# Kernel tuning notes

Measured on AMD Instinct MI355X. Metric: run time of the kernel, lower is better.

Reference implementation:

```python
import jax, jax.numpy as jnp
import numpy as np

B, S, E, H = 64, 512, 1024, 1024

def setup_inputs() -> dict:
    key = jax.random.key(0)
    k1, k2, k3, k4, k5 = jax.random.split(key, 5)
    emben_x = jax.random.normal(k1, (B, S, E), dtype=jnp.float32)
    sW = 1.0 / np.sqrt(E)
    sU = 1.0 / np.sqrt(H)
    W_w = jax.random.uniform(k2, (H, E), jnp.float32, -sW, sW)
    W_b = jax.random.uniform(k3, (H,), jnp.float32, -sW, sW)
    U_w = jax.random.uniform(k4, (H, H), jnp.float32, -sU, sU)
    U_b = jax.random.uniform(k5, (H,), jnp.float32, -sU, sU)
    return {"emben_x": emben_x, "W_w": W_w, "W_b": W_b, "U_w": U_w, "U_b": U_b}

def reference(emben_x, W_w, W_b, U_w, U_b):
    # Precompute input projection for all timesteps in one big GEMM: [B,S,H]
    wx = jnp.einsum('bse,he->bsh', emben_x, W_w) + W_b

    def step(t, wx_t):
        # h3 = tanh(W x_t + b_W + t); t_new = U h3 + b_U
        h3 = jnp.tanh(wx_t + t)
        t_new = h3 @ U_w.T + U_b
        return t_new, t_new

    t0 = jnp.zeros((emben_x.shape[0], U_w.shape[0]), dtype=emben_x.dtype)
    t_final, outs = jax.lax.scan(step, t0, jnp.swapaxes(wx, 0, 1))  # outs: [S,B,H]
    result1 = jnp.swapaxes(outs, 0, 1)  # [B,S,H]
    return result1, t_final
```

## Files before the change

kernel.cpp:

```cpp
#include <hip/hip_runtime.h>
#include <hip/hip_bf16.h>
#include <math.h>

#define RB 64
#define RS 512
#define RE 1024
#define RH 1024
#define BSH ((size_t)RB * RS * RH)

#define NBLK 256

typedef __attribute__((ext_vector_type(8))) __bf16 bf16x8;
typedef __attribute__((ext_vector_type(4))) float  f32x4;

__device__ __forceinline__ bf16x8 cvt8(f32x4 a, f32x4 b) {
    bf16x8 r;
    r[0] = (__bf16)a[0]; r[1] = (__bf16)a[1];
    r[2] = (__bf16)a[2]; r[3] = (__bf16)a[3];
    r[4] = (__bf16)b[0]; r[5] = (__bf16)b[1];
    r[6] = (__bf16)b[2]; r[7] = (__bf16)b[3];
    return r;
}

__device__ __forceinline__ bf16x8 ld_frag_agent(const unsigned long long* p) {
    union { unsigned long long u[2]; bf16x8 v; } r;
    r.u[0] = __hip_atomic_load(p,     __ATOMIC_RELAXED, __HIP_MEMORY_SCOPE_AGENT);
    r.u[1] = __hip_atomic_load(p + 1, __ATOMIC_RELAXED, __HIP_MEMORY_SCOPE_AGENT);
    return r.v;
}
__device__ __forceinline__ void st_bf16_agent(__bf16* p, float v) {
    union { __bf16 b; unsigned short s; } u;
    u.b = (__bf16)v;
    __hip_atomic_store(reinterpret_cast<unsigned short*>(p), u.s,
                       __ATOMIC_RELAXED, __HIP_MEMORY_SCOPE_AGENT);
}

__global__ void init_flags_k(unsigned* flags) {
    if (threadIdx.x < NBLK) flags[threadIdx.x] = 0u;
}

#define WBK  64
#define LDST 72

__global__ __launch_bounds__(256) void wx_gemm(
    const float* __restrict__ X,
    const float* __restrict__ Ww,
    const float* __restrict__ Wb,
    float* __restrict__ Out)
{
    __shared__ __align__(16) __bf16 As[128 * LDST];
    __shared__ __align__(16) __bf16 Bs[128 * LDST];

    const int tid  = threadIdx.x;
    const int lane = tid & 63;
    const int wave = tid >> 6;
    const int m0   = blockIdx.y * 128;
    const int n0   = blockIdx.x * 128;
    const int wm   = (wave >> 1) * 64;
    const int wn   = (wave & 1) * 64;

    const int sk   = (tid & 7) * 8;
    const int srow = tid >> 3;

    f32x4 acc[4][4];
#pragma unroll
    for (int i = 0; i < 4; ++i)
#pragma unroll
        for (int j = 0; j < 4; ++j) acc[i][j] = (f32x4){0.f, 0.f, 0.f, 0.f};

    for (int kc = 0; kc < RE; kc += WBK) {
#pragma unroll
        for (int rr = 0; rr < 128; rr += 32) {
            const float* xp = X + (size_t)(m0 + srow + rr) * RE + kc + sk;
            *reinterpret_cast<bf16x8*>(&As[(srow + rr) * LDST + sk]) =
                cvt8(*reinterpret_cast<const f32x4*>(xp),
                     *reinterpret_cast<const f32x4*>(xp + 4));
            const float* wp = Ww + (size_t)(n0 + srow + rr) * RE + kc + sk;
            *reinterpret_cast<bf16x8*>(&Bs[(srow + rr) * LDST + sk]) =
                cvt8(*reinterpret_cast<const f32x4*>(wp),
                     *reinterpret_cast<const f32x4*>(wp + 4));
        }
        __syncthreads();

#pragma unroll
        for (int ks = 0; ks < 2; ++ks) {
            bf16x8 af[4], bfr[4];
#pragma unroll
            for (int i = 0; i < 4; ++i) {
                af[i]  = *reinterpret_cast<const bf16x8*>(
                    &As[(wm + i * 16 + (lane & 15)) * LDST + ks * 32 + (lane >> 4) * 8]);
                bfr[i] = *reinterpret_cast<const bf16x8*>(
                    &Bs[(wn + i * 16 + (lane & 15)) * LDST + ks * 32 + (lane >> 4) * 8]);
            }
#pragma unroll
            for (int i = 0; i < 4; ++i)
#pragma unroll
                for (int j = 0; j < 4; ++j)
                    acc[i][j] = __builtin_amdgcn_mfma_f32_16x16x32_bf16(
                        af[i], bfr[j], acc[i][j], 0, 0, 0);
        }
        __syncthreads();
    }

    const int col = lane & 15, rbase = (lane >> 4) * 4;
#pragma unroll
    for (int j = 0; j < 4; ++j) {
        const int n = n0 + wn + j * 16 + col;
        const float bias = Wb[n];
#pragma unroll
        for (int i = 0; i < 4; ++i) {
#pragma unroll
            for (int r = 0; r < 4; ++r) {
                const int m = m0 + wm + i * 16 + rbase + r;
                Out[(size_t)m * RH + n] = acc[i][j][r] + bias;
            }
        }
    }
}

__global__ __launch_bounds__(128) void rnn_scan(
    const float* __restrict__ Uw,
    const float* __restrict__ Ub,
    float* Out,
    __bf16* hbuf,
    unsigned* flags)
{
    __shared__ float red[2][2][256];

    const int tid  = threadIdx.x;
    const int lane = tid & 63;
    const int wave = tid >> 6;
    const int bid  = blockIdx.x;
    const int cg   = bid >> 2;
    const int rg   = bid & 3;
    const int col0 = cg * 16;
    const int row0 = rg * 16;
    const int slot = rg * 64 + cg;

    bf16x8 ufr[16];
    {
        const float* up = Uw + (size_t)(col0 + (lane & 15)) * RH
                        + 512 * wave + ((lane >> 4) * 8);
#pragma unroll
        for (int j = 0; j < 16; ++j)
            ufr[j] = cvt8(*reinterpret_cast<const f32x4*>(up + j * 32),
                          *reinterpret_cast<const f32x4*>(up + j * 32 + 4));
    }

    const int e0row = row0 + (tid >> 4);
    const int e1row = e0row + 8;
    const int ecol  = col0 + (tid & 15);
    const float ub  = Ub[ecol];

    {
        const float w0 = Out[(size_t)e0row * RS * RH + ecol];
        const float w1 = Out[(size_t)e1row * RS * RH + ecol];
        st_bf16_agent(hbuf + e0row * RH + ecol, tanhf(w0));
        st_bf16_agent(hbuf + e1row * RH + ecol, tanhf(w1));
    }
    __syncthreads();
    if (tid == 0)
        __hip_atomic_store(&flags[slot], 1u,
                           __ATOMIC_RELAXED, __HIP_MEMORY_SCOPE_AGENT);

    const int arow  = row0 + (lane & 15);
    const int kbase = 512 * wave + (lane >> 4) * 8;
    const unsigned* myflags = flags + rg * 64;

    for (int t = 0; t < RS; ++t) {
        const __bf16* cur = hbuf + (size_t)(t & 1) * (RB * RH);
        __bf16*       nxt = hbuf + (size_t)((t + 1) & 1) * (RB * RH);
        const unsigned long long* cp =
            reinterpret_cast<const unsigned long long*>(cur)
            + ((size_t)arow * RH + kbase) / 4;

        float wn0 = 0.f, wn1 = 0.f;
        if (t < RS - 1) {
            wn0 = Out[(size_t)e0row * RS * RH + (size_t)(t + 1) * RH + ecol];
            wn1 = Out[(size_t)e1row * RS * RH + (size_t)(t + 1) * RH + ecol];
        }

        const unsigned tgt = (unsigned)(t + 1);
        while (true) {
            const unsigned f = __hip_atomic_load(&myflags[lane],
                                                 __ATOMIC_RELAXED,
                                                 __HIP_MEMORY_SCOPE_AGENT);
            if (__all(f >= tgt)) break;
            __builtin_amdgcn_s_sleep(1);
        }
        __builtin_amdgcn_sched_barrier(0);
        asm volatile("" ::: "memory");

        bf16x8 x[16];
#pragma unroll
        for (int f = 0; f < 16; ++f)
            x[f] = ld_frag_agent(cp + f * 8);

        f32x4 ac0 = (f32x4){0.f, 0.f, 0.f, 0.f};
        f32x4 ac1 = ac0, ac2 = ac0, ac3 = ac0;
#pragma unroll
        for (int f = 0; f < 16; f += 4) {
            ac0 = __builtin_amdgcn_mfma_f32_16x16x32_bf16(x[f + 0], ufr[f + 0], ac0, 0, 0, 0);
            ac1 = __builtin_amdgcn_mfma_f32_16x16x32_bf16(x[f + 1], ufr[f + 1], ac1, 0, 0, 0);
            ac2 = __builtin_amdgcn_mfma_f32_16x16x32_bf16(x[f + 2], ufr[f + 2], ac2, 0, 0, 0);
            ac3 = __builtin_amdgcn_mfma_f32_16x16x32_bf16(x[f + 3], ufr[f + 3], ac3, 0, 0, 0);
        }
        const f32x4 acc = (ac0 + ac1) + (ac2 + ac3);

        {
            float* rb = red[t & 1][wave];
#pragma unroll
            for (int r = 0; r < 4; ++r)
                rb[((lane >> 4) * 4 + r) * 16 + (lane & 15)] = acc[r];
        }
        __syncthreads();
        const float* r0 = red[t & 1][0];
        const float* r1 = red[t & 1][1];
        const float v0 = r0[tid]       + r1[tid]       + ub;
        const float v1 = r0[tid + 128] + r1[tid + 128] + ub;

        const size_t o0 = (size_t)e0row * RS * RH + (size_t)t * RH + ecol;
        const size_t o1 = (size_t)e1row * RS * RH + (size_t)t * RH + ecol;
        if (t == RS - 1) {
            Out[o0] = v0;
            Out[o1] = v1;
            Out[BSH + (size_t)e0row * RH + ecol] = v0;
            Out[BSH + (size_t)e1row * RH + ecol] = v1;
        } else {
            st_bf16_agent(nxt + e0row * RH + ecol, tanhf(wn0 + v0));
            st_bf16_agent(nxt + e1row * RH + ecol, tanhf(wn1 + v1));
            __syncthreads();
            if (tid == 0)
                __hip_atomic_store(&flags[slot], (unsigned)(t + 2),
                                   __ATOMIC_RELAXED, __HIP_MEMORY_SCOPE_AGENT);
            Out[o0] = v0;
            Out[o1] = v1;
        }
    }
}

extern "C" void kernel_launch(void* const* d_in, const int* in_sizes, int n_in,
                              void* d_out, int out_size, void* d_ws, size_t ws_size,
                              hipStream_t stream)
{
    const float* X  = (const float*)d_in[0];
    const float* Ww = (const float*)d_in[1];
    const float* Wb = (const float*)d_in[2];
    const float* Uw = (const float*)d_in[3];
    const float* Ub = (const float*)d_in[4];
    float* Out = (float*)d_out;

    __bf16* hbuf = (__bf16*)d_ws;
    unsigned* flags = (unsigned*)((char*)d_ws + (size_t)2 * RB * RH * sizeof(__bf16));

    hipLaunchKernelGGL(init_flags_k, dim3(1), dim3(256), 0, stream, flags);
    hipLaunchKernelGGL(wx_gemm, dim3(RH / 128, (RB * RS) / 128), dim3(256), 0, stream,
                       X, Ww, Wb, Out);
    hipLaunchKernelGGL(rnn_scan, dim3(NBLK), dim3(128), 0, stream,
                       Uw, Ub, Out, hbuf, flags);
}
```

Baseline: 2.245 ms.

## Replace per-step flag barrier with timestep-tagged hidden-state words in RNN scan

Adds a new scan kernel in which each hidden value is stored as a 32-bit word that packs the bf16 value with the timestep in the upper half. Consumers spin until every word they need carries the expected tag, so the separate flag handshake between producer and consumer blocks goes away. The block also grows to 4 waves splitting K four ways, with a shared-memory reduction. The cost is twice the bytes of hidden-state traffic and a full re-read whenever a tag check fails. The old flag-based path is kept as a fallback for when the workspace is too small.

```diff
diff --git a/kernel.cpp b/kernel.cpp
--- a/kernel.cpp
+++ b/kernel.cpp
@@ -33,6 +33,12 @@
     u.b = (__bf16)v;
     __hip_atomic_store(reinterpret_cast<unsigned short*>(p), u.s,
                        __ATOMIC_RELAXED, __HIP_MEMORY_SCOPE_AGENT);
+}
+
+__global__ __launch_bounds__(256) void init_tags_k(unsigned* tbuf) {
+    const int i = blockIdx.x * 256 + threadIdx.x;
+    tbuf[i]         = 0xFFFF0000u;
+    tbuf[i + 65536] = 0xFFFF0000u;
 }
 
 __global__ void init_flags_k(unsigned* flags) {
@@ -118,7 +124,135 @@
     }
 }
 
-__global__ __launch_bounds__(128) void rnn_scan(
+__global__ __launch_bounds__(256) void rnn_scan_tag(
+    const float* __restrict__ Uw,
+    const float* __restrict__ Ub,
+    float* Out,
+    unsigned* tbuf)
+{
+    __shared__ float red[2][4 * 256];
+    __shared__ float ubs[16];
+
+    const int tid  = threadIdx.x;
+    const int lane = tid & 63;
+    const int wave = tid >> 6;
+    const int bid  = blockIdx.x;
+    const int cg   = bid >> 2;
+    const int rg   = bid & 3;
+    const int col0 = cg * 16;
+    const int row0 = rg * 16;
+
+    bf16x8 ufr[8];
+    {
+        const float* up = Uw + (size_t)(col0 + (lane & 15)) * RH
+                        + 256 * wave + ((lane >> 4) * 8);
+#pragma unroll
+        for (int j = 0; j < 8; ++j)
+            ufr[j] = cvt8(*reinterpret_cast<const f32x4*>(up + j * 32),
+                          *reinterpret_cast<const f32x4*>(up + j * 32 + 4));
+    }
+    if (tid < 16) ubs[tid] = Ub[col0 + tid];
+
+    const int erow = row0 + (tid >> 4);
+    const int ecol = col0 + (tid & 15);
+
+    {
+        const float w = Out[(size_t)erow * RS * RH + ecol];
+        union { __bf16 b; unsigned short s; } u; u.b = (__bf16)tanhf(w);
+        __hip_atomic_store(&tbuf[(size_t)erow * RH + ecol], (unsigned)u.s,
+                           __ATOMIC_RELAXED, __HIP_MEMORY_SCOPE_AGENT);
+    }
+    float wn_cur = Out[(size_t)erow * RS * RH + (size_t)1 * RH + ecol];
+
+    const int arow  = row0 + (lane & 15);
+    const int kbase = 256 * wave + (lane >> 4) * 8;
+
+    for (int t = 0; t < RS; ++t) {
+        const unsigned* cur = tbuf + (size_t)(t & 1) * (RB * RH);
+        unsigned*       nxt = tbuf + (size_t)((t + 1) & 1) * (RB * RH);
+        const unsigned long long* cp =
+            reinterpret_cast<const unsigned long long*>(cur)
+            + ((size_t)arow * RH + kbase) / 2;
+
+        const unsigned long long half = ((unsigned long long)(unsigned)t) << 16;
+        const unsigned long long rep  = half | (half << 32);
+        const unsigned long long hm   = 0xFFFF0000FFFF0000ull;
+
+        while (true) {
+            const unsigned long long s =
+                __hip_atomic_load(cp, __ATOMIC_RELAXED, __HIP_MEMORY_SCOPE_AGENT);
+            if (__all(((s ^ rep) & hm) == 0ull)) break;
+            __builtin_amdgcn_s_sleep(1);
+        }
+
+        unsigned long long q[32];
+        while (true) {
+#pragma unroll
+            for (int f = 0; f < 8; ++f)
+#pragma unroll
+                for (int i = 0; i < 4; ++i)
+                    q[f * 4 + i] = __hip_atomic_load(cp + (size_t)f * 16 + i,
+                                                     __ATOMIC_RELAXED,
+                                                     __HIP_MEMORY_SCOPE_AGENT);
+            unsigned long long bad = 0;
+#pragma unroll
+            for (int j = 0; j < 32; ++j) { q[j] ^= rep; bad |= (q[j] & hm); }
+            if (__all(bad == 0ull)) break;
+            __builtin_amdgcn_s_sleep(2);
+        }
+
+        bf16x8 xf[8];
+#pragma unroll
+        for (int f = 0; f < 8; ++f) {
+            union { unsigned u[4]; bf16x8 v; } w;
+#pragma unroll
+            for (int i = 0; i < 4; ++i) {
+                const unsigned long long y = q[f * 4 + i];
+                const unsigned lo = (unsigned)y;
+                const unsigned hi = (unsigned)(y >> 32);
+                w.u[i] = lo | (hi << 16);
+            }
+            xf[f] = w.v;
+        }
+
+        f32x4 ac0 = (f32x4){0.f, 0.f, 0.f, 0.f};
+        f32x4 ac1 = ac0, ac2 = ac0, ac3 = ac0;
+        ac0 = __builtin_amdgcn_mfma_f32_16x16x32_bf16(xf[0], ufr[0], ac0, 0, 0, 0);
+        ac1 = __builtin_amdgcn_mfma_f32_16x16x32_bf16(xf[1], ufr[1], ac1, 0, 0, 0);
+        ac2 = __builtin_amdgcn_mfma_f32_16x16x32_bf16(xf[2], ufr[2], ac2, 0, 0, 0);
+        ac3 = __builtin_amdgcn_mfma_f32_16x16x32_bf16(xf[3], ufr[3], ac3, 0, 0, 0);
+        ac0 = __builtin_amdgcn_mfma_f32_16x16x32_bf16(xf[4], ufr[4], ac0, 0, 0, 0);
+        ac1 = __builtin_amdgcn_mfma_f32_16x16x32_bf16(xf[5], ufr[5], ac1, 0, 0, 0);
+        ac2 = __builtin_amdgcn_mfma_f32_16x16x32_bf16(xf[6], ufr[6], ac2, 0, 0, 0);
+        ac3 = __builtin_amdgcn_mfma_f32_16x16x32_bf16(xf[7], ufr[7], ac3, 0, 0, 0);
+        const f32x4 acc = (ac0 + ac1) + (ac2 + ac3);
+
+        float* rb = red[t & 1];
+#pragma unroll
+        for (int r = 0; r < 4; ++r)
+            rb[wave * 256 + ((lane >> 4) * 4 + r) * 16 + (lane & 15)] = acc[r];
+        __syncthreads();
+
+        const float v = rb[tid] + rb[256 + tid] + rb[512 + tid] + rb[768 + tid]
+                      + ubs[tid & 15];
+        const size_t oidx = (size_t)erow * RS * RH + (size_t)t * RH + ecol;
+        if (t == RS - 1) {
+            Out[oidx] = v;
+            Out[BSH + (size_t)erow * RH + ecol] = v;
+        } else {
+            const float h = tanhf(wn_cur + v);
+            union { __bf16 b; unsigned short s; } u; u.b = (__bf16)h;
+            const unsigned tv = ((unsigned)(t + 1) << 16) | (unsigned)u.s;
+            __hip_atomic_store(&nxt[(size_t)erow * RH + ecol], tv,
+                               __ATOMIC_RELAXED, __HIP_MEMORY_SCOPE_AGENT);
+            Out[oidx] = v;
+            if (t < RS - 2)
+                wn_cur = Out[(size_t)erow * RS * RH + (size_t)(t + 2) * RH + ecol];
+        }
+    }
+}
+
+__global__ __launch_bounds__(128) void rnn_scan_flags(
     const float* __restrict__ Uw,
     const float* __restrict__ Ub,
     float* Out,
@@ -250,12 +384,21 @@
     const float* Ub = (const float*)d_in[4];
     float* Out = (float*)d_out;
 
-    __bf16* hbuf = (__bf16*)d_ws;
-    unsigned* flags = (unsigned*)((char*)d_ws + (size_t)2 * RB * RH * sizeof(__bf16));
-
-    hipLaunchKernelGGL(init_flags_k, dim3(1), dim3(256), 0, stream, flags);
+    const size_t TAG_WS = (size_t)2 * RB * RH * sizeof(unsigned);
+
     hipLaunchKernelGGL(wx_gemm, dim3(RH / 128, (RB * RS) / 128), dim3(256), 0, stream,
                        X, Ww, Wb, Out);
-    hipLaunchKernelGGL(rnn_scan, dim3(NBLK), dim3(128), 0, stream,
-                       Uw, Ub, Out, hbuf, flags);
-}
+
+    if (ws_size >= TAG_WS) {
+        unsigned* tbuf = (unsigned*)d_ws;
+        hipLaunchKernelGGL(init_tags_k, dim3(256), dim3(256), 0, stream, tbuf);
+        hipLaunchKernelGGL(rnn_scan_tag, dim3(NBLK), dim3(256), 0, stream,
+                           Uw, Ub, Out, tbuf);
+    } else {
+        __bf16* hbuf = (__bf16*)d_ws;
+        unsigned* flags = (unsigned*)((char*)d_ws + (size_t)2 * RB * RH * sizeof(__bf16));
+        hipLaunchKernelGGL(init_flags_k, dim3(1), dim3(256), 0, stream, flags);
+        hipLaunchKernelGGL(rnn_scan_flags, dim3(NBLK), dim3(128), 0, stream,
+                           Uw, Ub, Out, hbuf, flags);
+    }
+}
```

Result: slower. 2.856 ms (+27.2%).
